# Kernel tuning notes

Measured on AMD Instinct MI355X. Metric: run time of the kernel, lower is better.

## Reference

```python
import jax, jax.numpy as jnp
import numpy as np

N_HEADS, N_LEVELS, N_POINTS, D_MODEL = 8, 4, 4, 256
HEAD_DIM = D_MODEL // N_HEADS
SHAPES = [(96, 96), (48, 48), (24, 24), (12, 12)]


def setup_inputs() -> dict:
    key = jax.random.key(0)
    ks = jax.random.split(key, 9)
    shapes_np = np.asarray(SHAPES, dtype=np.int32)
    lengths = shapes_np[:, 0] * shapes_np[:, 1]
    Len = int(lengths.sum())  # 12240
    B = 1
    level_start = np.concatenate([[0], np.cumsum(lengths)[:-1]]).astype(np.int32)
    return {
        "query": jax.random.normal(ks[0], (B, Len, D_MODEL), jnp.float32),
        "reference_points": jax.random.uniform(ks[1], (B, Len, 2), jnp.float32),
        "input_flatten": jax.random.normal(ks[2], (B, Len, D_MODEL), jnp.float32),
        "spatial_shapes": jnp.asarray(shapes_np),
        "level_start_index": jnp.asarray(level_start),
        "W_off": jax.random.normal(ks[3], (D_MODEL, N_HEADS * N_LEVELS * N_POINTS * 2), jnp.float32) * 0.01,
        "b_off": jax.random.normal(ks[4], (N_HEADS * N_LEVELS * N_POINTS * 2,), jnp.float32) * 0.01,
        "W_attn": jax.random.normal(ks[5], (D_MODEL, N_HEADS * N_LEVELS * N_POINTS), jnp.float32) * 0.02,
        "b_attn": jnp.zeros((N_HEADS * N_LEVELS * N_POINTS,), jnp.float32),
        "W_out": jax.random.normal(ks[6], (D_MODEL, D_MODEL), jnp.float32) * 0.02,
        "b_out": jnp.zeros((D_MODEL,), jnp.float32),
    }


def _bilinear_gather(feat, x, y, H, W):
    """feat: [B,nH,H*W,D]; x,y: [B,nH,S] pixel coords. Zero padding, align_corners=False."""
    x0 = jnp.floor(x)
    y0 = jnp.floor(y)
    wx1 = x - x0
    wy1 = y - y0
    wx0 = 1.0 - wx1
    wy0 = 1.0 - wy1
    x0i = x0.astype(jnp.int32)
    y0i = y0.astype(jnp.int32)

    def corner(ix, iy):
        valid = (ix >= 0) & (ix < W) & (iy >= 0) & (iy < H)
        idx = jnp.clip(iy, 0, H - 1) * W + jnp.clip(ix, 0, W - 1)
        g = jnp.take_along_axis(feat, idx[..., None], axis=2)  # [B,nH,S,D]
        return g * valid[..., None].astype(feat.dtype)

    return (corner(x0i, y0i) * (wx0 * wy0)[..., None]
            + corner(x0i + 1, y0i) * (wx1 * wy0)[..., None]
            + corner(x0i, y0i + 1) * (wx0 * wy1)[..., None]
            + corner(x0i + 1, y0i + 1) * (wx1 * wy1)[..., None])


def _ms_deform_core(value, shapes_np, loc, attn):
    """value: [B,Len_in,nH,D]; loc: [B,LQ,nH,nL,nP,2]; attn: [B,LQ,nH,nL,nP]."""
    B, LQ = loc.shape[0], loc.shape[1]
    lengths = [int(h) * int(w) for h, w in shapes_np]
    starts = np.concatenate([[0], np.cumsum(lengths)])
    out = jnp.zeros((B, N_HEADS, LQ, HEAD_DIM), value.dtype)
    for lvl, (H, W) in enumerate(shapes_np):
        H, W = int(H), int(W)
        feat = value[:, starts[lvl]:starts[lvl + 1]].transpose(0, 2, 1, 3)  # [B,nH,HW,D]
        l = loc[:, :, :, lvl]  # [B,LQ,nH,nP,2]
        x = (l[..., 0] * W - 0.5).transpose(0, 2, 1, 3).reshape(B, N_HEADS, LQ * N_POINTS)
        y = (l[..., 1] * H - 0.5).transpose(0, 2, 1, 3).reshape(B, N_HEADS, LQ * N_POINTS)
        samp = _bilinear_gather(feat, x, y, H, W).reshape(B, N_HEADS, LQ, N_POINTS, HEAD_DIM)
        w = attn[:, :, :, lvl].transpose(0, 2, 1, 3)  # [B,nH,LQ,nP]
        out = out + (samp * w[..., None]).sum(axis=3)
    return out.transpose(0, 2, 1, 3).reshape(B, LQ, N_HEADS * HEAD_DIM)


def reference(query, reference_points, input_flatten, spatial_shapes, level_start_index,
              W_off, b_off, W_attn, b_attn, W_out, b_out):
    B, LQ, C = query.shape
    shapes_np = np.asarray(spatial_shapes)  # static per-level (H,W)
    off = (query @ W_off + b_off).reshape(B, LQ, N_HEADS, N_LEVELS, N_POINTS, 2)
    attn = jax.nn.softmax((query @ W_attn + b_attn).reshape(B, LQ, N_HEADS, N_LEVELS * N_POINTS), axis=-1)
    attn = attn.reshape(B, LQ, N_HEADS, N_LEVELS, N_POINTS)
    # offset_normalizer = (W, H) per level
    norm = jnp.asarray(np.stack([shapes_np[:, 1], shapes_np[:, 0]], -1), dtype=query.dtype)
    loc = reference_points[:, :, None, None, None, :] + off / norm[None, None, None, :, None, :]
    value = input_flatten.reshape(B, -1, N_HEADS, HEAD_DIM)
    out = _ms_deform_core(value, shapes_np, loc, attn)
    return out @ W_out + b_out
```

## Files before the change

kernel.cpp:

```cpp
#include <hip/hip_runtime.h>
#include <hip/hip_bf16.h>
#include <math.h>

constexpr int D_MODEL  = 256;
constexpr int N_HEADS  = 8;

typedef __attribute__((ext_vector_type(8))) short bf16x8;
typedef __attribute__((ext_vector_type(4))) float f32x4;

__device__ __forceinline__ void gld_lds16(const void* gsrc, void* ldst) {
    __builtin_amdgcn_global_load_lds(
        (const __attribute__((address_space(1))) unsigned int*)gsrc,
        (__attribute__((address_space(3))) unsigned int*)ldst, 16, 0, 0);
}

__global__ __launch_bounds__(256) void convert_kernel(
    const float* __restrict__ q,
    const float* __restrict__ Woff,
    const float* __restrict__ Wattn,
    const float* __restrict__ Wout,
    const float* __restrict__ value,
    __hip_bfloat16* __restrict__ qbf,
    __hip_bfloat16* __restrict__ wt,
    float* __restrict__ vt,
    int M, int Lv)
{
    int t = blockIdx.x * 256 + threadIdx.x;
    int nq4 = M * 64;
    if (t < nq4) {
        float4 v = reinterpret_cast<const float4*>(q)[t];
        union { __hip_bfloat16 h[4]; ushort4 u; } cv;
        cv.h[0] = __float2bfloat16(v.x);
        cv.h[1] = __float2bfloat16(v.y);
        cv.h[2] = __float2bfloat16(v.z);
        cv.h[3] = __float2bfloat16(v.w);
        reinterpret_cast<ushort4*>(qbf)[t] = cv.u;
        return;
    }
    int t2 = t - nq4;
    if (t2 < 640 * 256) {
        int c = t2 >> 8, k = t2 & 255;
        float val = (c < 256) ? Woff[k * 256 + c]
                  : (c < 384) ? Wattn[k * 128 + (c - 256)]
                              : Wout[k * 256 + (c - 384)];
        wt[c * 256 + k] = __float2bfloat16(val);
        return;
    }
    int t3 = t2 - 640 * 256;
    if (t3 < Lv * 64) {
        int pix = t3 >> 6;
        int c4  = (t3 & 63) * 4;
        int h   = c4 >> 5, d = c4 & 31;
        float4 v = reinterpret_cast<const float4*>(value)[t3];
        *reinterpret_cast<float4*>(vt + (size_t)h * Lv * 32 + (size_t)pix * 32 + d) = v;
    }
}

template <int EPI>
__global__ __launch_bounds__(256) void gemm_mfma(
    const __hip_bfloat16* __restrict__ Abf,
    const __hip_bfloat16* __restrict__ Wt,
    int wrow0,
    const float* __restrict__ ba,
    const float* __restrict__ bb,
    const float* __restrict__ refpts,
    float* __restrict__ out0,
    float* __restrict__ out1,
    int M)
{
    __shared__ __align__(16) char smem[128 * 68 * 4];
    char*  A_lds = smem;
    char*  B_lds = smem + 16384;
    float* C_lds = (float*)smem;

    const int tid = threadIdx.x;
    const int w = tid >> 6, l = tid & 63;
    const int m0 = blockIdx.y * 128;
    const int n0 = blockIdx.x * 64;

    const char* Asrc = (const char*)Abf;
    const char* Wsrc = (const char*)(Wt + (size_t)(wrow0 + n0) * 256);

    f32x4 acc[2][4] = {};

    const int lr8 = l >> 3, l7 = l & 7;

    for (int k0 = 0; k0 < 512; k0 += 128) {
#pragma unroll
        for (int i = 0; i < 4; ++i) {
            int chunk = (w << 2) + i;
            int row = (chunk << 3) + lr8;
            int m = m0 + row; m = m < M ? m : (M - 1);
            gld_lds16(Asrc + (size_t)m * 512 + k0 + ((l7 ^ (row & 7)) << 4),
                      A_lds + (chunk << 10));
        }
#pragma unroll
        for (int i = 0; i < 2; ++i) {
            int chunk = (w << 1) + i;
            int row = (chunk << 3) + lr8;
            gld_lds16(Wsrc + (size_t)row * 512 + k0 + ((l7 ^ (row & 7)) << 4),
                      B_lds + (chunk << 10));
        }
        __syncthreads();

#pragma unroll
        for (int kk = 0; kk < 2; ++kk) {
            bf16x8 av[2], bv[4];
#pragma unroll
            for (int mf = 0; mf < 2; ++mf) {
                int arow = (w << 5) + (mf << 4) + (l & 15);
                int acb = ((kk << 6) + ((l >> 4) << 4)) ^ ((arow & 7) << 4);
                av[mf] = *(const bf16x8*)(A_lds + arow * 128 + acb);
            }
#pragma unroll
            for (int nf = 0; nf < 4; ++nf) {
                int brow = (nf << 4) + (l & 15);
                int bcb = ((kk << 6) + ((l >> 4) << 4)) ^ ((brow & 7) << 4);
                bv[nf] = *(const bf16x8*)(B_lds + brow * 128 + bcb);
            }
#pragma unroll
            for (int mf = 0; mf < 2; ++mf)
#pragma unroll
                for (int nf = 0; nf < 4; ++nf)
                    acc[mf][nf] = __builtin_amdgcn_mfma_f32_16x16x32_bf16(
                        av[mf], bv[nf], acc[mf][nf], 0, 0, 0);
        }
        __syncthreads();
    }

#pragma unroll
    for (int mf = 0; mf < 2; ++mf)
#pragma unroll
        for (int nf = 0; nf < 4; ++nf) {
            int col = (nf << 4) + (l & 15);
            int rbase = (w << 5) + (mf << 4) + ((l >> 4) << 2);
#pragma unroll
            for (int j = 0; j < 4; ++j)
                C_lds[(rbase + j) * 68 + col] = acc[mf][nf][j];
        }
    __syncthreads();

    if (EPI == 0 || n0 < 256) {
#pragma unroll
        for (int r2 = 0; r2 < 2; ++r2) {
            int row = (r2 << 6) + (tid >> 2);
            int q = m0 + row;
            if (q >= M) continue;
            float rx = 0.f, ry = 0.f;
            if (EPI == 1) { rx = refpts[q * 2]; ry = refpts[q * 2 + 1]; }
#pragma unroll
            for (int g = 0; g < 4; ++g) {
                int col = ((tid & 3) << 4) + (g << 2);
                float4 v  = *(float4*)&C_lds[row * 68 + col];
                float4 b4 = *(const float4*)&ba[n0 + col];
                if (EPI == 0) {
                    v.x += b4.x; v.y += b4.y; v.z += b4.z; v.w += b4.w;
                } else {
                    int c = n0 + col;
                    float rn = 1.0f / (float)(96 >> ((c >> 3) & 3));
                    v.x = rx + (v.x + b4.x) * rn;
                    v.y = ry + (v.y + b4.y) * rn;
                    v.z = rx + (v.z + b4.z) * rn;
                    v.w = ry + (v.w + b4.w) * rn;
                }
                *(float4*)&out0[(size_t)q * 256 + n0 + col] = v;
            }
        }
    } else {
        for (int u = tid; u < 512; u += 256) {
            int row = u >> 2, hh = u & 3;
            int q = m0 + row;
            if (q >= M) continue;
            int cg = (n0 - 256) + (hh << 4);
            float s[16];
            float mx = -1e30f;
#pragma unroll
            for (int i = 0; i < 16; ++i) {
                s[i] = C_lds[row * 68 + (hh << 4) + i] + bb[cg + i];
                mx = fmaxf(mx, s[i]);
            }
            float sum = 0.f;
#pragma unroll
            for (int i = 0; i < 16; ++i) { s[i] = __expf(s[i] - mx); sum += s[i]; }
            float inv = 1.0f / sum;
#pragma unroll
            for (int g = 0; g < 4; ++g) {
                float4 v = make_float4(s[g*4]*inv, s[g*4+1]*inv, s[g*4+2]*inv, s[g*4+3]*inv);
                *(float4*)&out1[(size_t)q * 128 + cg + (g << 2)] = v;
            }
        }
    }
}

__global__ __launch_bounds__(256, 8) void sample_kernel(
    const float* __restrict__ loc,
    const float* __restrict__ attn,
    const float* __restrict__ vt,
    __hip_bfloat16* __restrict__ core,
    int M, int Lv)
{
    const int h    = blockIdx.x & 7;
    const int q0   = (blockIdx.x >> 3) << 5;
    const int unit = threadIdx.x >> 3;
    const int d4   = threadIdx.x & 7;
    const int q    = q0 + unit;
    if (q >= M) return;

    const float4* locq4 = reinterpret_cast<const float4*>(loc  + (size_t)q * 256 + h * 32);
    const float4* attq4 = reinterpret_cast<const float4*>(attn + (size_t)q * 128 + h * 16);
    const float*  plane = vt + (size_t)h * Lv * 32 + d4 * 4;

    float4 acc = make_float4(0.f, 0.f, 0.f, 0.f);

#pragma unroll 1
    for (int lvl = 0; lvl < 4; ++lvl) {
        const int Wl = 96 >> lvl;
        const int start = 12288 - (12288 >> (2 * lvl));
        const float fW = (float)Wl;
        const int rowstride = Wl * 32;
        const float* feat = plane + (size_t)start * 32;

        float4 lp0 = locq4[lvl * 2 + 0];
        float4 lp1 = locq4[lvl * 2 + 1];
        float4 aw  = attq4[lvl];

        const float lxs[4] = {lp0.x, lp0.z, lp1.x, lp1.z};
        const float lys[4] = {lp0.y, lp0.w, lp1.y, lp1.w};
        const float aws[4] = {aw.x, aw.y, aw.z, aw.w};

#pragma unroll
        for (int p = 0; p < 4; ++p) {
            float x = lxs[p] * fW - 0.5f;
            float y = lys[p] * fW - 0.5f;
            float wgt = aws[p];

            float x0f = floorf(x);
            float y0f = floorf(y);
            float wx1 = x - x0f, wy1 = y - y0f;
            float wx0 = 1.f - wx1, wy0 = 1.f - wy1;
            int ix = (int)x0f;
            int iy = (int)y0f;

            float wxv0 = ((unsigned)ix       < (unsigned)Wl) ? wx0 : 0.f;
            float wxv1 = ((unsigned)(ix + 1) < (unsigned)Wl) ? wx1 : 0.f;
            float wyv0 = (((unsigned)iy       < (unsigned)Wl) ? wy0 : 0.f) * wgt;
            float wyv1 = (((unsigned)(iy + 1) < (unsigned)Wl) ? wy1 : 0.f) * wgt;

            int ix0 = min(max(ix,     0), Wl - 1);
            int ix1 = min(max(ix + 1, 0), Wl - 1);
            int iy0 = min(max(iy,     0), Wl - 1);
            int iy1 = min(max(iy + 1, 0), Wl - 1);

            const float* row0 = feat + (size_t)iy0 * rowstride;
            const float* row1 = feat + (size_t)iy1 * rowstride;
            float4 v00 = *reinterpret_cast<const float4*>(&row0[ix0 * 32]);
            float4 v10 = *reinterpret_cast<const float4*>(&row0[ix1 * 32]);
            float4 v01 = *reinterpret_cast<const float4*>(&row1[ix0 * 32]);
            float4 v11 = *reinterpret_cast<const float4*>(&row1[ix1 * 32]);

            float w00 = wxv0 * wyv0, w10 = wxv1 * wyv0;
            float w01 = wxv0 * wyv1, w11 = wxv1 * wyv1;

            acc.x = fmaf(v00.x, w00, acc.x); acc.x = fmaf(v10.x, w10, acc.x);
            acc.x = fmaf(v01.x, w01, acc.x); acc.x = fmaf(v11.x, w11, acc.x);
            acc.y = fmaf(v00.y, w00, acc.y); acc.y = fmaf(v10.y, w10, acc.y);
            acc.y = fmaf(v01.y, w01, acc.y); acc.y = fmaf(v11.y, w11, acc.y);
            acc.z = fmaf(v00.z, w00, acc.z); acc.z = fmaf(v10.z, w10, acc.z);
            acc.z = fmaf(v01.z, w01, acc.z); acc.z = fmaf(v11.z, w11, acc.z);
            acc.w = fmaf(v00.w, w00, acc.w); acc.w = fmaf(v10.w, w10, acc.w);
            acc.w = fmaf(v01.w, w01, acc.w); acc.w = fmaf(v11.w, w11, acc.w);
        }
    }

    union { __hip_bfloat16 h4[4]; ushort4 u4; } st;
    st.h4[0] = __float2bfloat16(acc.x);
    st.h4[1] = __float2bfloat16(acc.y);
    st.h4[2] = __float2bfloat16(acc.z);
    st.h4[3] = __float2bfloat16(acc.w);
    *reinterpret_cast<ushort4*>(core + ((size_t)q * 256 + h * 32 + d4 * 4)) = st.u4;
}

extern "C" void kernel_launch(void* const* d_in, const int* in_sizes, int n_in,
                              void* d_out, int out_size, void* d_ws, size_t ws_size,
                              hipStream_t stream)
{
    const float* query  = (const float*)d_in[0];
    const float* refp   = (const float*)d_in[1];
    const float* value  = (const float*)d_in[2];
    const float* W_off  = (const float*)d_in[5];
    const float* b_off  = (const float*)d_in[6];
    const float* W_attn = (const float*)d_in[7];
    const float* b_attn = (const float*)d_in[8];
    const float* W_out  = (const float*)d_in[9];
    const float* b_out  = (const float*)d_in[10];
    float* out = (float*)d_out;

    const int M  = in_sizes[0] / D_MODEL;
    const int Lv = in_sizes[2] / D_MODEL;

    float* loc  = (float*)d_ws;
    float* attn = loc + (size_t)M * 256;
    __hip_bfloat16* qbf = (__hip_bfloat16*)(attn + (size_t)M * 128);
    __hip_bfloat16* wt  = qbf + (size_t)M * 256;
    float* vt = (float*)(wt + 640 * 256);
    __hip_bfloat16* core = qbf;

    dim3 blk(256);
    const int mblocks = (M + 127) / 128;

    int convthreads = M * 64 + 640 * 256 + Lv * 64;
    hipLaunchKernelGGL(convert_kernel, dim3((convthreads + 255) / 256), blk, 0, stream,
                       query, W_off, W_attn, W_out, value, qbf, wt, vt, M, Lv);

    hipLaunchKernelGGL((gemm_mfma<1>), dim3(6, mblocks), blk, 0, stream,
                       qbf, wt, 0, b_off, b_attn, refp, loc, attn, M);

    const int qchunks = (M + 31) / 32;
    hipLaunchKernelGGL(sample_kernel, dim3(qchunks * 8), blk, 0, stream,
                       loc, attn, vt, core, M, Lv);

    hipLaunchKernelGGL((gemm_mfma<0>), dim3(4, mblocks), blk, 0, stream,
                       core, wt, 384, b_out, nullptr, nullptr, out, nullptr, M);
}
```

Measured before the change: 74.76 us.

## Store value planes in bf16 and distribute sampling setup across lanes via ds_swizzle

The value tensor is now converted to bf16 during the layout transpose, which halves gather traffic in the sampling kernel. The sampling kernel is restructured so each of the 8 lanes of a query computes bilinear weights and offsets for 2 of the 16 points. Lanes then exchange these via ds_swizzle broadcasts, removing the redundant per-lane coordinate math and the level loop. The trade-off is reduced precision on sampled values plus extra cross-lane swizzle instructions.

```diff
diff --git a/kernel.cpp b/kernel.cpp
--- a/kernel.cpp
+++ b/kernel.cpp
@@ -22,7 +22,7 @@
     const float* __restrict__ value,
     __hip_bfloat16* __restrict__ qbf,
     __hip_bfloat16* __restrict__ wt,
-    float* __restrict__ vt,
+    __hip_bfloat16* __restrict__ vt,
     int M, int Lv)
 {
     int t = blockIdx.x * 256 + threadIdx.x;
@@ -52,7 +52,12 @@
         int c4  = (t3 & 63) * 4;
         int h   = c4 >> 5, d = c4 & 31;
         float4 v = reinterpret_cast<const float4*>(value)[t3];
-        *reinterpret_cast<float4*>(vt + (size_t)h * Lv * 32 + (size_t)pix * 32 + d) = v;
+        union { __hip_bfloat16 h4[4]; ushort4 u; } cv;
+        cv.h4[0] = __float2bfloat16(v.x);
+        cv.h4[1] = __float2bfloat16(v.y);
+        cv.h4[2] = __float2bfloat16(v.z);
+        cv.h4[3] = __float2bfloat16(v.w);
+        *reinterpret_cast<ushort4*>(vt + (size_t)h * Lv * 32 + (size_t)pix * 32 + d) = cv.u;
     }
 }
 
@@ -192,92 +197,137 @@
     }
 }
 
+template <int IMM>
+__device__ __forceinline__ float swzf(float v) {
+    return __int_as_float(__builtin_amdgcn_ds_swizzle(__float_as_int(v), IMM));
+}
+template <int IMM>
+__device__ __forceinline__ int swzi(int v) {
+    return __builtin_amdgcn_ds_swizzle(v, IMM);
+}
+
+template <int P>
+__device__ __forceinline__ void do_point(
+    const float wv[2][4], const int ov[2][4], const char* planeB,
+    float& a0, float& a1, float& a2, float& a3)
+{
+    constexpr int S   = P & 1;
+    constexpr int IMM = ((P >> 1) << 5) | 0x18;
+
+    float w00 = swzf<IMM>(wv[S][0]);
+    float w10 = swzf<IMM>(wv[S][1]);
+    float w01 = swzf<IMM>(wv[S][2]);
+    float w11 = swzf<IMM>(wv[S][3]);
+    int o00 = swzi<IMM>(ov[S][0]);
+    int o10 = swzi<IMM>(ov[S][1]);
+    int o01 = swzi<IMM>(ov[S][2]);
+    int o11 = swzi<IMM>(ov[S][3]);
+
+    uint2 u00 = *(const uint2*)(planeB + o00);
+    uint2 u10 = *(const uint2*)(planeB + o10);
+    uint2 u01 = *(const uint2*)(planeB + o01);
+    uint2 u11 = *(const uint2*)(planeB + o11);
+
+    a0 = fmaf(__uint_as_float(u00.x << 16),         w00, a0);
+    a1 = fmaf(__uint_as_float(u00.x & 0xffff0000u), w00, a1);
+    a2 = fmaf(__uint_as_float(u00.y << 16),         w00, a2);
+    a3 = fmaf(__uint_as_float(u00.y & 0xffff0000u), w00, a3);
+    a0 = fmaf(__uint_as_float(u10.x << 16),         w10, a0);
+    a1 = fmaf(__uint_as_float(u10.x & 0xffff0000u), w10, a1);
+    a2 = fmaf(__uint_as_float(u10.y << 16),         w10, a2);
+    a3 = fmaf(__uint_as_float(u10.y & 0xffff0000u), w10, a3);
+    a0 = fmaf(__uint_as_float(u01.x << 16),         w01, a0);
+    a1 = fmaf(__uint_as_float(u01.x & 0xffff0000u), w01, a1);
+    a2 = fmaf(__uint_as_float(u01.y << 16),         w01, a2);
+    a3 = fmaf(__uint_as_float(u01.y & 0xffff0000u), w01, a3);
+    a0 = fmaf(__uint_as_float(u11.x << 16),         w11, a0);
+    a1 = fmaf(__uint_as_float(u11.x & 0xffff0000u), w11, a1);
+    a2 = fmaf(__uint_as_float(u11.y << 16),         w11, a2);
+    a3 = fmaf(__uint_as_float(u11.y & 0xffff0000u), w11, a3);
+}
+
 __global__ __launch_bounds__(256, 8) void sample_kernel(
     const float* __restrict__ loc,
     const float* __restrict__ attn,
-    const float* __restrict__ vt,
+    const __hip_bfloat16* __restrict__ vt,
     __hip_bfloat16* __restrict__ core,
     int M, int Lv)
 {
     const int h    = blockIdx.x & 7;
     const int q0   = (blockIdx.x >> 3) << 5;
     const int unit = threadIdx.x >> 3;
-    const int d4   = threadIdx.x & 7;
+    const int k    = threadIdx.x & 7;
     const int q    = q0 + unit;
     if (q >= M) return;
 
-    const float4* locq4 = reinterpret_cast<const float4*>(loc  + (size_t)q * 256 + h * 32);
-    const float4* attq4 = reinterpret_cast<const float4*>(attn + (size_t)q * 128 + h * 16);
-    const float*  plane = vt + (size_t)h * Lv * 32 + d4 * 4;
-
-    float4 acc = make_float4(0.f, 0.f, 0.f, 0.f);
-
-#pragma unroll 1
-    for (int lvl = 0; lvl < 4; ++lvl) {
-        const int Wl = 96 >> lvl;
-        const int start = 12288 - (12288 >> (2 * lvl));
-        const float fW = (float)Wl;
-        const int rowstride = Wl * 32;
-        const float* feat = plane + (size_t)start * 32;
-
-        float4 lp0 = locq4[lvl * 2 + 0];
-        float4 lp1 = locq4[lvl * 2 + 1];
-        float4 aw  = attq4[lvl];
-
-        const float lxs[4] = {lp0.x, lp0.z, lp1.x, lp1.z};
-        const float lys[4] = {lp0.y, lp0.w, lp1.y, lp1.w};
-        const float aws[4] = {aw.x, aw.y, aw.z, aw.w};
-
-#pragma unroll
-        for (int p = 0; p < 4; ++p) {
-            float x = lxs[p] * fW - 0.5f;
-            float y = lys[p] * fW - 0.5f;
-            float wgt = aws[p];
-
-            float x0f = floorf(x);
-            float y0f = floorf(y);
-            float wx1 = x - x0f, wy1 = y - y0f;
-            float wx0 = 1.f - wx1, wy0 = 1.f - wy1;
-            int ix = (int)x0f;
-            int iy = (int)y0f;
-
-            float wxv0 = ((unsigned)ix       < (unsigned)Wl) ? wx0 : 0.f;
-            float wxv1 = ((unsigned)(ix + 1) < (unsigned)Wl) ? wx1 : 0.f;
-            float wyv0 = (((unsigned)iy       < (unsigned)Wl) ? wy0 : 0.f) * wgt;
-            float wyv1 = (((unsigned)(iy + 1) < (unsigned)Wl) ? wy1 : 0.f) * wgt;
-
-            int ix0 = min(max(ix,     0), Wl - 1);
-            int ix1 = min(max(ix + 1, 0), Wl - 1);
-            int iy0 = min(max(iy,     0), Wl - 1);
-            int iy1 = min(max(iy + 1, 0), Wl - 1);
-
-            const float* row0 = feat + (size_t)iy0 * rowstride;
-            const float* row1 = feat + (size_t)iy1 * rowstride;
-            float4 v00 = *reinterpret_cast<const float4*>(&row0[ix0 * 32]);
-            float4 v10 = *reinterpret_cast<const float4*>(&row0[ix1 * 32]);
-            float4 v01 = *reinterpret_cast<const float4*>(&row1[ix0 * 32]);
-            float4 v11 = *reinterpret_cast<const float4*>(&row1[ix1 * 32]);
-
-            float w00 = wxv0 * wyv0, w10 = wxv1 * wyv0;
-            float w01 = wxv0 * wyv1, w11 = wxv1 * wyv1;
-
-            acc.x = fmaf(v00.x, w00, acc.x); acc.x = fmaf(v10.x, w10, acc.x);
-            acc.x = fmaf(v01.x, w01, acc.x); acc.x = fmaf(v11.x, w11, acc.x);
-            acc.y = fmaf(v00.y, w00, acc.y); acc.y = fmaf(v10.y, w10, acc.y);
-            acc.y = fmaf(v01.y, w01, acc.y); acc.y = fmaf(v11.y, w11, acc.y);
-            acc.z = fmaf(v00.z, w00, acc.z); acc.z = fmaf(v10.z, w10, acc.z);
-            acc.z = fmaf(v01.z, w01, acc.z); acc.z = fmaf(v11.z, w11, acc.z);
-            acc.w = fmaf(v00.w, w00, acc.w); acc.w = fmaf(v10.w, w10, acc.w);
-            acc.w = fmaf(v01.w, w01, acc.w); acc.w = fmaf(v11.w, w11, acc.w);
-        }
-    }
+    const int lvl   = k >> 1;
+    const int Wl    = 96 >> lvl;
+    const int start = 12288 - (12288 >> (2 * lvl));
+    const float fW  = (float)Wl;
+    const int pil0  = (k & 1) << 1;
+
+    const float* lq = loc + (size_t)q * 256 + h * 32 + lvl * 8 + pil0 * 2;
+    float2 l01 = *(const float2*)lq;
+    float2 l23 = *(const float2*)(lq + 2);
+    float2 aw  = *(const float2*)(attn + (size_t)q * 128 + h * 16 + lvl * 4 + pil0);
+
+    float wv[2][4]; int ov[2][4];
+#pragma unroll
+    for (int s = 0; s < 2; ++s) {
+        float lx  = s ? l23.x : l01.x;
+        float ly  = s ? l23.y : l01.y;
+        float wgt = s ? aw.y  : aw.x;
+
+        float x = lx * fW - 0.5f;
+        float y = ly * fW - 0.5f;
+        float xf = floorf(x), yf = floorf(y);
+        float wx1 = x - xf, wy1 = y - yf;
+        float wx0 = 1.f - wx1, wy0 = 1.f - wy1;
+        int ix = (int)xf, iy = (int)yf;
+
+        float wxv0 = ((unsigned)ix       < (unsigned)Wl) ? wx0 : 0.f;
+        float wxv1 = ((unsigned)(ix + 1) < (unsigned)Wl) ? wx1 : 0.f;
+        float wyv0 = (((unsigned)iy       < (unsigned)Wl) ? wy0 : 0.f) * wgt;
+        float wyv1 = (((unsigned)(iy + 1) < (unsigned)Wl) ? wy1 : 0.f) * wgt;
+
+        int ix0 = min(max(ix,     0), Wl - 1);
+        int ix1 = min(max(ix + 1, 0), Wl - 1);
+        int iy0 = min(max(iy,     0), Wl - 1);
+        int iy1 = min(max(iy + 1, 0), Wl - 1);
+
+        int r0 = start + iy0 * Wl, r1 = start + iy1 * Wl;
+        wv[s][0] = wxv0 * wyv0;  ov[s][0] = (r0 + ix0) << 6;
+        wv[s][1] = wxv1 * wyv0;  ov[s][1] = (r0 + ix1) << 6;
+        wv[s][2] = wxv0 * wyv1;  ov[s][2] = (r1 + ix0) << 6;
+        wv[s][3] = wxv1 * wyv1;  ov[s][3] = (r1 + ix1) << 6;
+    }
+
+    const char* planeB = (const char*)vt + (size_t)h * Lv * 64 + k * 8;
+    float a0 = 0.f, a1 = 0.f, a2 = 0.f, a3 = 0.f;
+
+    do_point< 0>(wv, ov, planeB, a0, a1, a2, a3);
+    do_point< 1>(wv, ov, planeB, a0, a1, a2, a3);
+    do_point< 2>(wv, ov, planeB, a0, a1, a2, a3);
+    do_point< 3>(wv, ov, planeB, a0, a1, a2, a3);
+    do_point< 4>(wv, ov, planeB, a0, a1, a2, a3);
+    do_point< 5>(wv, ov, planeB, a0, a1, a2, a3);
+    do_point< 6>(wv, ov, planeB, a0, a1, a2, a3);
+    do_point< 7>(wv, ov, planeB, a0, a1, a2, a3);
+    do_point< 8>(wv, ov, planeB, a0, a1, a2, a3);
+    do_point< 9>(wv, ov, planeB, a0, a1, a2, a3);
+    do_point<10>(wv, ov, planeB, a0, a1, a2, a3);
+    do_point<11>(wv, ov, planeB, a0, a1, a2, a3);
+    do_point<12>(wv, ov, planeB, a0, a1, a2, a3);
+    do_point<13>(wv, ov, planeB, a0, a1, a2, a3);
+    do_point<14>(wv, ov, planeB, a0, a1, a2, a3);
+    do_point<15>(wv, ov, planeB, a0, a1, a2, a3);
 
     union { __hip_bfloat16 h4[4]; ushort4 u4; } st;
-    st.h4[0] = __float2bfloat16(acc.x);
-    st.h4[1] = __float2bfloat16(acc.y);
-    st.h4[2] = __float2bfloat16(acc.z);
-    st.h4[3] = __float2bfloat16(acc.w);
-    *reinterpret_cast<ushort4*>(core + ((size_t)q * 256 + h * 32 + d4 * 4)) = st.u4;
+    st.h4[0] = __float2bfloat16(a0);
+    st.h4[1] = __float2bfloat16(a1);
+    st.h4[2] = __float2bfloat16(a2);
+    st.h4[3] = __float2bfloat16(a3);
+    *reinterpret_cast<ushort4*>(core + ((size_t)q * 256 + h * 32 + k * 4)) = st.u4;
 }
 
 extern "C" void kernel_launch(void* const* d_in, const int* in_sizes, int n_in,
@@ -302,7 +352,7 @@
     float* attn = loc + (size_t)M * 256;
     __hip_bfloat16* qbf = (__hip_bfloat16*)(attn + (size_t)M * 128);
     __hip_bfloat16* wt  = qbf + (size_t)M * 256;
-    float* vt = (float*)(wt + 640 * 256);
+    __hip_bfloat16* vt  = wt + 640 * 256;
     __hip_bfloat16* core = qbf;
 
     dim3 blk(256);
```

New measurement: 68.21 us. 8.8% less time.
